# Kernel tuning notes

Hardware: AMD Instinct MI355X
Metric: run time of the kernel (lower is better)

## Reference

```python
import jax, jax.numpy as jnp
import numpy as np

NE, NT, NC, D, NR = 100000, 1024, 128, 128, 500
H, E, L_GCN = 8, 4, 2
B, DEG = 512, 8
NSRC = B * DEG
NNZ_E2T, NNZ_T2C, NNZ_E2C = 1000000, 50000, 500000
TAU, DECAY, CLW = 0.5, 1e-4, 0.1
N_NODES = NE + NT + NC


def setup_inputs() -> dict:
    ks = iter(jax.random.split(jax.random.key(0), 64))
    def n(shape, s=0.05):
        return jax.random.normal(next(ks), shape, jnp.float32) * s
    def ri(shape, hi):
        return jax.random.randint(next(ks), shape, 0, hi, jnp.int32)
    def u(shape):
        return jax.random.uniform(next(ks), shape, jnp.float32) * 0.01
    T = NT
    return {
        'entity_emb': n((NE, D)), 'type_emb': n((NT, D)), 'cluster_emb': n((NC, D)),
        'relation': n((NR, 2 * D)),
        'ln_g': jnp.ones((D,), jnp.float32), 'ln_b': jnp.zeros((D,), jnp.float32),
        'cl_w1': n((D, D)), 'cl_b1': jnp.zeros((D,), jnp.float32),
        'cl_w2': n((D, D)), 'cl_b2': jnp.zeros((D,), jnp.float32),
        'fc_w': n((2 * D, T)), 'fc_b': jnp.zeros((T,), jnp.float32),
        'wq': n((T, T)), 'bq': jnp.zeros((T,), jnp.float32),
        'wk': n((T, T)), 'bk': jnp.zeros((T,), jnp.float32),
        'wv': n((T, T)), 'bv': jnp.zeros((T,), jnp.float32),
        'wo': n((T, T)), 'bo': jnp.zeros((T,), jnp.float32),
        'gate_w': n((T, E)), 'exp_w': n((E, T, T)), 'exp_b': jnp.zeros((E, T), jnp.float32),
        'e2t_val': u((NNZ_E2T,)), 't2c_val': u((NNZ_T2C,)), 'e2c_val': u((NNZ_E2C,)),
        'e2t_row': ri((NNZ_E2T,), NE + NT), 'e2t_col': ri((NNZ_E2T,), NE + NT),
        't2c_row': ri((NNZ_T2C,), NT + NC), 't2c_col': ri((NNZ_T2C,), NT + NC),
        'e2c_row': ri((NNZ_E2C,), NE + NC), 'e2c_col': ri((NNZ_E2C,), NE + NC),
        'src_ids': ri((NSRC,), N_NODES), 'etype': ri((NSRC,), 2 * NR),
    }


def _light_gcn(ea, eb, row, col, val, na, nb):
    x = jnp.concatenate([ea, eb], axis=0)
    acc = x
    for _ in range(L_GCN):  # fixed small layer count
        x = jax.ops.segment_sum(val[:, None] * x[col], row, num_segments=na + nb)
        acc = acc + x
    m = acc / (L_GCN + 1)
    return m[:na], m[na:]


def _ln(x, g, b):
    mu = x.mean(-1, keepdims=True)
    var = x.var(-1, keepdims=True)
    return (x - mu) * jax.lax.rsqrt(var + 1e-5) * g + b


def _cl_loss(src1, src2, w1, b1, w2, b2):
    def proj(x):
        return jax.nn.elu(x @ w1 + b1) @ w2 + b2
    def norm(x):
        return x / jnp.maximum(jnp.linalg.norm(x, axis=1, keepdims=True), 1e-12)
    z1, z2 = norm(proj(src1)), norm(proj(src2))
    s11 = jnp.exp(z1 @ z1.T / TAU)   # [N,N]
    s12 = jnp.exp(z1 @ z2.T / TAU)
    s22 = jnp.exp(z2 @ z2.T / TAU)
    d12 = jnp.diag(s12)
    l1 = -jnp.log(d12 / (s11.sum(1) + s12.sum(1) - jnp.diag(s11)))
    l2 = -jnp.log(d12 / (s22.sum(1) + s12.sum(0) - jnp.diag(s22)))
    return ((l1 + l2) * 0.5).mean()


def _mha_moe(x, wq, bq, wk, bk, wv, bv, wo, bo, gate_w, exp_w, exp_b):
    # x: [B, DEG, T]; MHA over mailbox axis, then softmax-gated MoE, mean-pool.
    b, l, t = x.shape
    dh = t // H
    q = (x @ wq + bq).reshape(b, l, H, dh)
    k = (x @ wk + bk).reshape(b, l, H, dh)
    v = (x @ wv + bv).reshape(b, l, H, dh)
    attn = jax.nn.softmax(jnp.einsum('blhd,bmhd->bhlm', q, k) / jnp.sqrt(jnp.float32(dh)), axis=-1)
    o = jnp.einsum('bhlm,bmhd->blhd', attn, v).reshape(b, l, t) @ wo + bo
    gate = jax.nn.softmax(o @ gate_w, axis=-1)               # [B,L,E]
    eo = jnp.einsum('blt,etu->bleu', o, exp_w) + exp_b       # [B,L,E,T]
    moe = jnp.einsum('ble,blet->blt', gate, eo)
    return moe.mean(axis=1)                                  # [B,T]


def reference(entity_emb, type_emb, cluster_emb, relation, ln_g, ln_b,
              cl_w1, cl_b1, cl_w2, cl_b2, fc_w, fc_b,
              wq, bq, wk, bk, wv, bv, wo, bo, gate_w, exp_w, exp_b,
              e2t_val, t2c_val, e2c_val,
              e2t_row, e2t_col, t2c_row, t2c_col, e2c_row, e2c_col,
              src_ids, etype):
    e2t_e, e2t_t = _light_gcn(entity_emb, type_emb, e2t_row, e2t_col, e2t_val, NE, NT)
    t2c_t, t2c_c = _light_gcn(type_emb, cluster_emb, t2c_row, t2c_col, t2c_val, NT, NC)
    e2c_e, e2c_c = _light_gcn(entity_emb, cluster_emb, e2c_row, e2c_col, e2c_val, NE, NC)
    # with_norm=True path; dropout is eval-mode identity
    e2t_e, e2t_t = _ln(e2t_e, ln_g, ln_b), _ln(e2t_t, ln_g, ln_b)
    t2c_t, t2c_c = _ln(t2c_t, ln_g, ln_b), _ln(t2c_c, ln_g, ln_b)
    e2c_e, e2c_c = _ln(e2c_e, ln_g, ln_b), _ln(e2c_c, ln_g, ln_b)
    node1 = jnp.concatenate([e2t_e, e2t_t, t2c_c], axis=0)
    node2 = jnp.concatenate([e2c_e, t2c_t, e2c_c], axis=0)
    src1 = node1[src_ids]   # [NSRC, D]
    src2 = node2[src_ids]
    cl = _cl_loss(src1, src2, cl_w1, cl_b1, cl_w2, cl_b2)
    src = jnp.concatenate([src1, src2], axis=-1)  # [NSRC, 2D]
    sign = jnp.where(etype >= NR, -1.0, 1.0).astype(jnp.float32)[:, None]
    rel = relation[etype % NR] * sign
    emb_loss = DECAY * ((src ** 2).sum() + (rel ** 2).sum()) * 0.5 / rel.shape[0]
    aux_loss = CLW * cl + emb_loss
    # update_all: u_add_e message, regular mailbox [B, DEG, 2D]
    msg = jax.nn.relu(src + rel).reshape(B, DEG, 2 * D)
    predict = msg @ fc_w + fc_b                                  # [B, DEG, NT]
    predict = _mha_moe(predict, wq, bq, wk, bk, wv, bv, wo, bo, gate_w, exp_w, exp_b)
    out = jax.nn.sigmoid(predict)                                # [B, NT]
    return out, aux_loss
```

## Files before the change

### kernel.cpp

```cpp
#include <hip/hip_runtime.h>
#include <hip/hip_bf16.h>
#include <cmath>

constexpr int cNE = 100000, cNT = 1024, cNC = 128, cD = 128, cNR = 500;
constexpr int cB = 512, cNSRC = 4096, cT = 1024, cE = 4;
constexpr int cNNZ_E2T = 1000000, cNNZ_T2C = 50000, cNNZ_E2C = 500000;
constexpr float cDECAY = 1e-4f, cCLW = 0.1f;
constexpr int cNN_E2T = cNE + cNT;
constexpr int cNN_E2C = cNE + cNC;
constexpr int cNN_T2C = cNT + cNC;

constexpr size_t F_S1   = 0;
constexpr size_t F_S2   = F_S1 + 524288;
constexpr size_t F_PT   = F_S2 + 524288;
constexpr size_t F_Z1   = F_PT + 524288;
constexpr size_t F_Z2   = F_Z1 + 524288;
constexpr size_t F_MSG  = F_Z2 + 524288;
constexpr size_t F_GATE = F_MSG + 524288;
constexpr size_t F_SCAL = F_GATE + 16384;
constexpr size_t F_RS   = F_SCAL + 64;
constexpr size_t F_D11  = F_RS + 16384;
constexpr size_t F_D12  = F_D11 + 4096;
constexpr size_t F_D22  = F_D12 + 4096;
constexpr size_t F_U    = F_D22 + 4096;
// ... 209 lines not shown
}

__global__ __launch_bounds__(256) void k_gather_slot(
    const int* __restrict__ rowptr, const int* __restrict__ cols, const float* __restrict__ vals,
    const ushort* __restrict__ x1, const int* __restrict__ rep,
    ushort* __restrict__ outc) {
  int i = blockIdx.x * 4 + (threadIdx.x >> 6);
  if (i >= cNSRC) return;
  int r = rep[i];
  if (r < 0) return;
  int lane = threadIdx.x & 63;
  int p0 = rowptr[r], p1 = rowptr[r + 1];
  float ax = 0.f, ay = 0.f;
  int p = p0;
  for (; p + 4 <= p1; p += 4) {
    int c0 = cols[p], c1 = cols[p + 1], c2 = cols[p + 2], c3 = cols[p + 3];
    float v0 = vals[p], v1 = vals[p + 1], v2 = vals[p + 2], v3 = vals[p + 3];
    ushort2 x0 = *reinterpret_cast<const ushort2*>(x1 + (size_t)c0 * cD + lane * 2);
    ushort2 x1v = *reinterpret_cast<const ushort2*>(x1 + (size_t)c1 * cD + lane * 2);
    ushort2 x2 = *reinterpret_cast<const ushort2*>(x1 + (size_t)c2 * cD + lane * 2);
    ushort2 x3 = *reinterpret_cast<const ushort2*>(x1 + (size_t)c3 * cD + lane * 2);
    ax += v0 * bf2f(x0.x) + v1 * bf2f(x1v.x) + v2 * bf2f(x2.x) + v3 * bf2f(x3.x);
    ay += v0 * bf2f(x0.y) + v1 * bf2f(x1v.y) + v2 * bf2f(x2.y) + v3 * bf2f(x3.y);
  }
  for (; p < p1; ++p) {
    int c = cols[p];
    float v = vals[p];
    ushort2 x = *reinterpret_cast<const ushort2*>(x1 + (size_t)c * cD + lane * 2);
    ax += v * bf2f(x.x); ay += v * bf2f(x.y);
  }
  ushort2 o; o.x = f2bf(ax); o.y = f2bf(ay);
  *reinterpret_cast<ushort2*>(outc + (size_t)i * cD + lane * 2) = o;
}

__global__ __launch_bounds__(256) void k_gather_bf(
    const int* __restrict__ rowptr, const int* __restrict__ cols, const float* __restrict__ vals,
    const ushort* __restrict__ x1, int nrows, ushort* __restrict__ out) {
  int r = blockIdx.x * 4 + (threadIdx.x >> 6);
  if (r >= nrows) return;
  int lane = threadIdx.x & 63;
  int p0 = rowptr[r], p1 = rowptr[r + 1];
  float ax = 0.f, ay = 0.f;
  for (int p = p0; p < p1; ++p) {
    int c = cols[p];
    float v = vals[p];
    ushort2 x = *reinterpret_cast<const ushort2*>(x1 + (size_t)c * cD + lane * 2);
    ax += v * bf2f(x.x); ay += v * bf2f(x.y);
  }
  ushort2 o; o.x = f2bf(ax); o.y = f2bf(ay);
  *reinterpret_cast<ushort2*>(out + (size_t)r * cD + lane * 2) = o;
}

__global__ __launch_bounds__(128) void gather_ln(
    const int* __restrict__ ids, int mode,
    const float* __restrict__ ea, const float* __restrict__ eb, int na,
    const ushort* __restrict__ x1, const ushort* __restrict__ x2, const int* __restrict__ slot,
    const float* __restrict__ g, const float* __restrict__ bia, float* __restrict__ dst) {
  __shared__ float shx[2], shy[2];
  int i = blockIdx.x;
  int tid = threadIdx.x;
  int id = ids[i];
  int node = mapNode(mode, id);
  if (node < 0) return;
  const float* x0 = (node < na) ? (ea + (size_t)node * cD) : (eb + (size_t)(node - na) * cD);
  int xi2 = slot ? slot[node] : node;
  float a = (x0[tid] + bf2f(x1[(size_t)node * cD + tid]) + bf2f(x2[(size_t)xi2 * cD + tid]))
            * (1.0f / 3.0f);
  float sx = a, sy = a * a;
#pragma unroll
  for (int off = 32; off > 0; off >>= 1) {
    sx += __shfl_xor(sx, off);
    sy += __shfl_xor(sy, off);
  }
  if ((tid & 63) == 0) { shx[tid >> 6] = sx; shy[tid >> 6] = sy; }
  __syncthreads();
  float s  = shx[0] + shx[1];
  float ss = shy[0] + shy[1];
  float mu = s * (1.0f / 128.0f);
  float var = ss * (1.0f / 128.0f) - mu * mu;
  float y = (a - mu) * rsqrtf(var + 1e-5f) * g[tid] + bia[tid];
  dst[(size_t)i * cD + tid] = y;
}

__global__ __launch_bounds__(256) void gemm_bf(
    const ushort* __restrict__ A, const ushort* __restrict__ Bt,
    int N, int K, const float* __restrict__ bias, ushort* __restrict__ Cbf, int epi) {
  __shared__ ushort As[128 * 40];
  __shared__ ushort Bs[128 * 40];
  const int bx = blockIdx.x, by = blockIdx.y;
  const int t = threadIdx.x;
  const int wv = t >> 6, lane = t & 63;
  const int wr = (wv >> 1) * 64, wc = (wv & 1) * 64;
  const int srow = t >> 1, shalf = t & 1;
  const ushort* Ag = A + (size_t)(by * 128 + srow) * K + shalf * 16;
  const ushort* Bg = Bt + (size_t)(bx * 128 + srow) * K + shalf * 16;
  uint4 ra0 = *reinterpret_cast<const uint4*>(Ag);
  uint4 ra1 = *reinterpret_cast<const uint4*>(Ag + 8);
  uint4 rb0 = *reinterpret_cast<const uint4*>(Bg);
  uint4 rb1 = *reinterpret_cast<const uint4*>(Bg + 8);
  f32x4 acc[4][4];
  const f32x4 z4 = {0.f, 0.f, 0.f, 0.f};
#pragma unroll
  for (int i = 0; i < 4; ++i)
#pragma unroll
    for (int j = 0; j < 4; ++j) acc[i][j] = z4;
  const int la = lane & 15, lk = (lane >> 4) * 8;
  const int sdst = srow * 40 + shalf * 16;
  for (int kt = 0; kt < K; kt += 32) {
    __syncthreads();
    *reinterpret_cast<uint4*>(&As[sdst])     = ra0;
    *reinterpret_cast<uint4*>(&As[sdst + 8]) = ra1;
    *reinterpret_cast<uint4*>(&Bs[sdst])     = rb0;
    *reinterpret_cast<uint4*>(&Bs[sdst + 8]) = rb1;
    __syncthreads();
    if (kt + 32 < K) {
      ra0 = *reinterpret_cast<const uint4*>(Ag + kt + 32);
      ra1 = *reinterpret_cast<const uint4*>(Ag + kt + 40);
      rb0 = *reinterpret_cast<const uint4*>(Bg + kt + 32);
      rb1 = *reinterpret_cast<const uint4*>(Bg + kt + 40);
    }
    short8v af[4], bfr[4];
#pragma unroll
    for (int i = 0; i < 4; ++i)
      af[i] = *reinterpret_cast<const short8v*>(&As[(wr + i * 16 + la) * 40 + lk]);
#pragma unroll
    for (int j = 0; j < 4; ++j)
      bfr[j] = *reinterpret_cast<const short8v*>(&Bs[(wc + j * 16 + la) * 40 + lk]);
#pragma unroll
    for (int i = 0; i < 4; ++i)
#pragma unroll
      for (int j = 0; j < 4; ++j)
        acc[i][j] = __builtin_amdgcn_mfma_f32_16x16x32_bf16(af[i], bfr[j], acc[i][j], 0, 0, 0);
  }
  const int r0 = by * 128 + wr + (lane >> 4) * 4;
  const int c0 = bx * 128 + wc + la;
#pragma unroll
  for (int i = 0; i < 4; ++i)
#pragma unroll
    for (int j = 0; j < 4; ++j) {
      int c = c0 + j * 16;
      float bv = bias[c];
#pragma unroll
      for (int q = 0; q < 4; ++q) {
        int r = r0 + i * 16 + q;
        float v = acc[i][j][q] + bv;
        if (epi == 1) v = (v > 0.0f) ? v : expm1f(v);
        Cbf[(size_t)r * N + c] = f2bf(v);
      }
    }
}

__global__ __launch_bounds__(256) void k_gate_pool(
    const ushort* __restrict__ o, const float* __restrict__ gw,
    ushort* __restrict__ ae, float* __restrict__ gsum) {
  __shared__ float os[8][1024];
  __shared__ float lg[8][4];
  __shared__ float gs[8][4];
  const int b = blockIdx.x, t = threadIdx.x;
  for (int u = t; u < 8192; u += 256) {
    int l = u >> 10, d = u & 1023;
    os[l][d] = bf2f(o[(size_t)(b * 8 + l) * 1024 + d]);
  }
  __syncthreads();
  {
    int p = t >> 3, sub = t & 7;
    int l = p >> 2, e = p & 3;
    float s = 0;
    for (int d = sub; d < 1024; d += 8) s += os[l][d] * gw[d * 4 + e];
    s += __shfl_down(s, 4, 8);
    s += __shfl_down(s, 2, 8);
    s += __shfl_down(s, 1, 8);
    if (sub == 0) lg[l][e] = s;
  }
  __syncthreads();
  if (t < 8) {
    float m = fmaxf(fmaxf(lg[t][0], lg[t][1]), fmaxf(lg[t][2], lg[t][3]));
    float e0 = expf(lg[t][0] - m), e1 = expf(lg[t][1] - m);
    float e2 = expf(lg[t][2] - m), e3 = expf(lg[t][3] - m);
    float inv = 1.0f / (e0 + e1 + e2 + e3);
    gs[t][0] = e0 * inv; gs[t][1] = e1 * inv;
    gs[t][2] = e2 * inv; gs[t][3] = e3 * inv;
  }
  __syncthreads();
  if (t < 4) {
    float g = 0;
#pragma unroll
    for (int l = 0; l < 8; ++l) g += gs[l][t];
    gsum[b * 4 + t] = g;
  }
#pragma unroll
  for (int rep = 0; rep < 4; ++rep) {
    int d = t + rep * 256;
    float a0 = 0, a1 = 0, a2 = 0, a3 = 0;
#pragma unroll
    for (int l = 0; l < 8; ++l) {
      float ov = os[l][d];
      a0 += gs[l][0] * ov; a1 += gs[l][1] * ov;
      a2 += gs[l][2] * ov; a3 += gs[l][3] * ov;
    }
    ae[(size_t)0 * 524288 + b * 1024 + d] = f2bf(a0);
    ae[(size_t)1 * 524288 + b * 1024 + d] = f2bf(a1);
    ae[(size_t)2 * 524288 + b * 1024 + d] = f2bf(a2);
    ae[(size_t)3 * 524288 + b * 1024 + d] = f2bf(a3);
  }
}

__global__ __launch_bounds__(256) void gemm_moe2(
    const ushort* __restrict__ AE, const ushort* __restrict__ Bt4,
    const float* __restrict__ expb, const float* __restrict__ gsum,
    float* __restrict__ out) {
  __shared__ ushort As[64 * 40];
  __shared__ ushort Bs[64 * 40];
  const int bx = blockIdx.x, by = blockIdx.y;
  const int t = threadIdx.x;
  const int wv = t >> 6, lane = t & 63;
  const int wr = (wv >> 1) * 32, wc = (wv & 1) * 32;
  const int srow = t >> 2, sq = t & 3;
  const int la = lane & 15, lk = (lane >> 4) * 8;
  const int sdst = srow * 40 + sq * 8;
  f32x4 acc[2][2];
  const f32x4 z4 = {0.f, 0.f, 0.f, 0.f};
  acc[0][0] = z4; acc[0][1] = z4; acc[1][0] = z4; acc[1][1] = z4;
  for (int e = 0; e < 4; ++e) {
    const ushort* Ag = AE + (size_t)e * 524288 + (size_t)(by * 64 + srow) * 1024 + sq * 8;
    const ushort* Bg = Bt4 + (size_t)e * 1048576 + (size_t)(bx * 64 + srow) * 1024 + sq * 8;
    uint4 ra = *reinterpret_cast<const uint4*>(Ag);
    uint4 rb = *reinterpret_cast<const uint4*>(Bg);
    for (int kt = 0; kt < 1024; kt += 32) {
      __syncthreads();
      *reinterpret_cast<uint4*>(&As[sdst]) = ra;
      *reinterpret_cast<uint4*>(&Bs[sdst]) = rb;
      __syncthreads();
      if (kt + 32 < 1024) {
        ra = *reinterpret_cast<const uint4*>(Ag + kt + 32);
        rb = *reinterpret_cast<const uint4*>(Bg + kt + 32);
      }
      short8v af[2], bfr[2];
#pragma unroll
      for (int i = 0; i < 2; ++i)
        af[i] = *reinterpret_cast<const short8v*>(&As[(wr + i * 16 + la) * 40 + lk]);
#pragma unroll
      for (int j = 0; j < 2; ++j)
        bfr[j] = *reinterpret_cast<const short8v*>(&Bs[(wc + j * 16 + la) * 40 + lk]);
#pragma unroll
      for (int i = 0; i < 2; ++i)
#pragma unroll
        for (int j = 0; j < 2; ++j)
          acc[i][j] = __builtin_amdgcn_mfma_f32_16x16x32_bf16(af[i], bfr[j], acc[i][j], 0, 0, 0);
    }
  }
  const int r0 = by * 64 + wr + (lane >> 4) * 4;
  const int c0 = bx * 64 + wc + la;
#pragma unroll
  for (int i = 0; i < 2; ++i)
#pragma unroll
    for (int q = 0; q < 4; ++q) {
      int r = r0 + i * 16 + q;
      float4 gv = *reinterpret_cast<const float4*>(gsum + r * 4);
#pragma unroll
      for (int j = 0; j < 2; ++j) {
        int c = c0 + j * 16;
        float bias = gv.x * expb[c] + gv.y * expb[1024 + c] +
                     gv.z * expb[2048 + c] + gv.w * expb[3072 + c];
        float s = (acc[i][j][q] + bias) * 0.125f;
        out[(size_t)r * 1024 + c] = 1.0f / (1.0f + expf(-s));
      }
    }
}

__global__ __launch_bounds__(256) void gram_sym(
    const ushort* __restrict__ W, float* __restrict__ rsum,
    float* __restrict__ d11, float* __restrict__ d12, float* __restrict__ d22) {
  __shared__ ushort As[128 * 40];
  __shared__ ushort Bs[128 * 40];
  int tt = blockIdx.x, bi = 0, cnt = 64;
  while (tt >= cnt) { tt -= cnt; ++bi; --cnt; }
  int bj = bi + tt;
  const bool diag = (bi == bj);
  const int t = threadIdx.x;
  const int wv = t >> 6, lane = t & 63;
  const int wr = (wv >> 1) * 64, wc = (wv & 1) * 64;
  const int srow = t >> 1, shalf = t & 1;
  const ushort* Ag = W + (size_t)(bi * 128 + srow) * 128 + shalf * 16;
  const ushort* Bg = W + (size_t)(bj * 128 + srow) * 128 + shalf * 16;
  uint4 ra0 = *reinterpret_cast<const uint4*>(Ag);
  uint4 ra1 = *reinterpret_cast<const uint4*>(Ag + 8);
  uint4 rb0 = *reinterpret_cast<const uint4*>(Bg);
  uint4 rb1 = *reinterpret_cast<const uint4*>(Bg + 8);
  f32x4 acc[4][4];
  const f32x4 z4 = {0.f, 0.f, 0.f, 0.f};
#pragma unroll
  for (int i = 0; i < 4; ++i)
#pragma unroll
    for (int j = 0; j < 4; ++j) acc[i][j] = z4;
  const int la = lane & 15, lk = (lane >> 4) * 8;
  const int sdst = srow * 40 + shalf * 16;
  for (int kt = 0; kt < 128; kt += 32) {
    __syncthreads();
    *reinterpret_cast<uint4*>(&As[sdst])     = ra0;
    *reinterpret_cast<uint4*>(&As[sdst + 8]) = ra1;
    *reinterpret_cast<uint4*>(&Bs[sdst])     = rb0;
    *reinterpret_cast<uint4*>(&Bs[sdst + 8]) = rb1;
    __syncthreads();
    if (kt + 32 < 128) {
      ra0 = *reinterpret_cast<const uint4*>(Ag + kt + 32);
      ra1 = *reinterpret_cast<const uint4*>(Ag + kt + 40);
      rb0 = *reinterpret_cast<const uint4*>(Bg + kt + 32);
      rb1 = *reinterpret_cast<const uint4*>(Bg + kt + 40);
    }
    short8v af[4], bfr[4];
#pragma unroll
    for (int i = 0; i < 4; ++i)
      af[i] = *reinterpret_cast<const short8v*>(&As[(wr + i * 16 + la) * 40 + lk]);
#pragma unroll
    for (int j = 0; j < 4; ++j)
      bfr[j] = *reinterpret_cast<const short8v*>(&Bs[(wc + j * 16 + la) * 40 + lk]);
#pragma unroll
    for (int i = 0; i < 4; ++i)
#pragma unroll
      for (int j = 0; j < 4; ++j)
        acc[i][j] = __builtin_amdgcn_mfma_f32_16x16x32_bf16(af[i], bfr[j], acc[i][j], 0, 0, 0);
  }
  const int r0 = bi * 128 + wr + (lane >> 4) * 4;
  const int c0 = bj * 128 + wc + la;
  constexpr float K2 = 2.8853900817779268f;
  float rs[4][4];
  float cs[4] = {0.f, 0.f, 0.f, 0.f};
#pragma unroll
  for (int i = 0; i < 4; ++i)
#pragma unroll
    for (int q = 0; q < 4; ++q) rs[i][q] = 0.f;
#pragma unroll
  for (int i = 0; i < 4; ++i)
#pragma unroll
    for (int j = 0; j < 4; ++j)
#pragma unroll
      for (int q = 0; q < 4; ++q) {
        int r = r0 + i * 16 + q;
        int c = c0 + j * 16;
        float e = exp2f(K2 * acc[i][j][q]);
        rs[i][q] += e;
        cs[j] += e;
        if (c == r)        { if (r < 4096) d11[r] = e; else d22[r - 4096] = e; }
        if (c == r + 4096) d12[r] = e;
      }
#pragma unroll
  for (int m = 1; m < 16; m <<= 1)
#pragma unroll
    for (int i = 0; i < 4; ++i)
#pragma unroll
      for (int q = 0; q < 4; ++q) rs[i][q] += __shfl_xor(rs[i][q], m);
  float* rowdst = rsum + ((bj >= 32) ? 8192 : 0);
  if (la == 0) {
#pragma unroll
    for (int i = 0; i < 4; ++i)
#pragma unroll
      for (int q = 0; q < 4; ++q) atomAdd(&rowdst[r0 + i * 16 + q], rs[i][q]);
  }
  if (!diag) {
#pragma unroll
    for (int j = 0; j < 4; ++j) {
      cs[j] += __shfl_xor(cs[j], 16);
      cs[j] += __shfl_xor(cs[j], 32);
    }
    float* coldst = rsum + ((bi >= 32) ? 8192 : 0);
    if ((lane >> 4) == 0) {
#pragma unroll
      for (int j = 0; j < 4; ++j) atomAdd(&coldst[c0 + j * 16], cs[j]);
    }
  }
}

__global__ __launch_bounds__(256) void cl_row(
    const float* __restrict__ rsum, const float* __restrict__ d11,
    const float* __restrict__ d12, const float* __restrict__ d22,
    float* __restrict__ cl_sum) {
  __shared__ float sh[256];
  int i = blockIdx.x * 256 + threadIdx.x;
  float denA = rsum[i] + rsum[8192 + i] - d11[i];
  float denB = rsum[8192 + 4096 + i] + rsum[4096 + i] - d22[i];
  float l = 0.5f * (logf(denA) + logf(denB)) - logf(d12[i]);
  float s = blockReduce256(l, sh, threadIdx.x);
  if (threadIdx.x == 0) atomAdd(cl_sum, s);
}

__global__ __launch_bounds__(256) void k_wt_bt(const float* __restrict__ W,
                                               ushort* __restrict__ Bt, int K, int N) {
  __shared__ float tile[32][33];
  int n0 = blockIdx.x * 32, k0 = blockIdx.y * 32;
  int tx = threadIdx.x & 31, ty = threadIdx.x >> 5;
#pragma unroll
  for (int i = 0; i < 4; ++i)
    tile[ty + 8 * i][tx] = W[(size_t)(k0 + ty + 8 * i) * N + n0 + tx];
  __syncthreads();
#pragma unroll
  for (int i = 0; i < 4; ++i)
    Bt[(size_t)(n0 + ty + 8 * i) * K + k0 + tx] = f2bf(tile[tx][ty + 8 * i]);
}

__global__ __launch_bounds__(256) void k_wt_bt_s(const float* __restrict__ Wbase,
                                                 ushort* __restrict__ Btbase, int K, int N) {
  __shared__ float tile[32][33];
  const float* W = Wbase + (size_t)blockIdx.z * K * N;
  ushort* Bt = Btbase + (size_t)blockIdx.z * K * N;
  int n0 = blockIdx.x * 32, k0 = blockIdx.y * 32;
  int tx = threadIdx.x & 31, ty = threadIdx.x >> 5;
#pragma unroll
  for (int i = 0; i < 4; ++i)
    tile[ty + 8 * i][tx] = W[(size_t)(k0 + ty + 8 * i) * N + n0 + tx];
  __syncthreads();
#pragma unroll
  for (int i = 0; i < 4; ++i)
    Bt[(size_t)(n0 + ty + 8 * i) * K + k0 + tx] = f2bf(tile[tx][ty + 8 * i]);
}

__global__ __launch_bounds__(256) void k_wt_bt3(const float* __restrict__ w0,
                                                const float* __restrict__ w1,
                                                const float* __restrict__ w2,
                                                ushort* __restrict__ Btbase, int K, int N) {
  __shared__ float tile[32][33];
  const float* W = (blockIdx.z == 0) ? w0 : (blockIdx.z == 1) ? w1 : w2;
  ushort* Bt = Btbase + (size_t)blockIdx.z * K * N;
  int n0 = blockIdx.x * 32, k0 = blockIdx.y * 32;
  int tx = threadIdx.x & 31, ty = threadIdx.x >> 5;
#pragma unroll
  for (int i = 0; i < 4; ++i)
    tile[ty + 8 * i][tx] = W[(size_t)(k0 + ty + 8 * i) * N + n0 + tx];
  __syncthreads();
#pragma unroll
  for (int i = 0; i < 4; ++i)
    Bt[(size_t)(n0 + ty + 8 * i) * K + k0 + tx] = f2bf(tile[tx][ty + 8 * i]);
}

__global__ __launch_bounds__(256) void k_post_s(
    const float* __restrict__ s1, const float* __restrict__ s2,
    const float* __restrict__ relation, const int* __restrict__ etype,
    ushort* __restrict__ sb, ushort* __restrict__ msg, float* __restrict__ emb_out) {
  __shared__ float sh[256];
  float part = 0.f;
  for (int idx = blockIdx.x * 256 + threadIdx.x; idx < 1048576; idx += 128 * 256) {
    float vs = (idx < 524288) ? s1[idx] : s2[idx - 524288];
    sb[idx] = f2bf(vs);
    int i = idx >> 8, j = idx & 255;
    int et = etype[i];
    float sign = (et >= cNR) ? -1.0f : 1.0f;
    float r = relation[(size_t)(et % cNR) * 256 + j];
    float s = (j < 128) ? s1[(size_t)i * 128 + j] : s2[(size_t)i * 128 + j - 128];
    msg[idx] = f2bf(fmaxf(s + r * sign, 0.0f));
    part += s * s + r * r;
  }
  float tot = blockReduce256(part, sh, threadIdx.x);
  if (threadIdx.x == 0) atomAdd(emb_out, tot);
}

__global__ __launch_bounds__(128) void rownorm_bf2(ushort* __restrict__ w) {
  __shared__ float sh[2];
  int i = blockIdx.x, tid = threadIdx.x;
  float v = bf2f(w[(size_t)i * cD + tid]);
  float ss = v * v;
#pragma unroll
  for (int off = 32; off > 0; off >>= 1) ss += __shfl_xor(ss, off);
  if ((tid & 63) == 0) sh[tid >> 6] = ss;
  __syncthreads();
  float n = fmaxf(sqrtf(sh[0] + sh[1]), 1e-12f);
  w[(size_t)i * cD + tid] = f2bf(v / n);
}
// ... 45 lines not shown
    o[(size_t)(b * 8 + ll) * 1024 + h * 128 + d] = f2bf(acc);
  }
}

__global__ void finalize_k(const float* __restrict__ scal, float* __restrict__ out_aux) {
  float cl = scal[0] * (1.0f / cNSRC);
  float emb = cDECAY * 0.5f * scal[1] * (1.0f / cNSRC);
  out_aux[0] = cCLW * cl + emb;
}

extern "C" void kernel_launch(void* const* d_in, const int* in_sizes, int n_in,
                              void* d_out, int out_size, void* d_ws, size_t ws_size,
                              hipStream_t stream) {
  (void)in_sizes; (void)n_in; (void)out_size; (void)ws_size;
  const float* entity   = (const float*)d_in[0];
  const float* type_e   = (const float*)d_in[1];
  const float* cluster  = (const float*)d_in[2];
  const float* relation = (const float*)d_in[3];
  const float* ln_g  = (const float*)d_in[4];
  const float* ln_b  = (const float*)d_in[5];
  const float* cl_w1 = (const float*)d_in[6];
  const float* cl_b1 = (const float*)d_in[7];
  const float* cl_w2 = (const float*)d_in[8];
  const float* cl_b2 = (const float*)d_in[9];
  const float* fc_w  = (const float*)d_in[10];
  const float* fc_b  = (const float*)d_in[11];
  const float* wq = (const float*)d_in[12];
  const float* bq = (const float*)d_in[13];
  const float* wk = (const float*)d_in[14];
  const float* bk = (const float*)d_in[15];
  const float* wv = (const float*)d_in[16];
  const float* bv = (const float*)d_in[17];
  const float* wo = (const float*)d_in[18];
  const float* bo = (const float*)d_in[19];
  const float* gate_w = (const float*)d_in[20];
  const float* exp_w  = (const float*)d_in[21];
  const float* exp_b  = (const float*)d_in[22];
  const float* e2t_val = (const float*)d_in[23];
  const float* t2c_val = (const float*)d_in[24];
  const float* e2c_val = (const float*)d_in[25];
  const int* e2t_row = (const int*)d_in[26];
  const int* e2t_col = (const int*)d_in[27];
  const int* t2c_row = (const int*)d_in[28];
  const int* t2c_col = (const int*)d_in[29];
  const int* e2c_row = (const int*)d_in[30];
  const int* e2c_col = (const int*)d_in[31];
  const int* src_ids = (const int*)d_in[32];
  const int* etype   = (const int*)d_in[33];

  float* ws = (float*)d_ws;
  float* S1 = ws + F_S1;
  float* S2 = ws + F_S2;
  ushort* Wbf = (ushort*)(ws + F_PT);
  ushort* P1bf = (ushort*)(ws + F_Z1);
  ushort* SBbf = (ushort*)(ws + F_Z2);
  ushort* MSGbf = (ushort*)(ws + F_MSG);
  float* GSUM = ws + F_GATE;
  float* SCAL = ws + F_SCAL;
  float* RS   = ws + F_RS;
  float* BQKV = ws + F_RS;
  float* D11  = ws + F_D11;
  float* D12  = ws + F_D12;
  float* D22  = ws + F_D22;
  ushort* X1F = (ushort*)(ws + G_X1F);
  ushort* X2C = (ushort*)(ws + G_X2C);
  int*   MARK = (int*)(ws + G_X2C);
  int*   SLOT = (int*)(ws + G_SLOT);
  int*   REP  = (int*)(ws + G_REP);
  int*   RP   = (int*)(ws + G_RP);
  int*   FILL = (int*)(ws + G_FILL);
  int*   COLS = (int*)(ws + G_COLS);
  float* VALS = ws + G_VALS;
  ushort* X1T = (ushort*)(ws + G_X1T);
  ushort* X2T = (ushort*)(ws + G_X2T);
  int*   BSUM = (int*)(ws + G_BSUM);
  ushort* EBF = (ushort*)(ws + G_EBF);
  ushort* TBF = (ushort*)(ws + G_TBF);
  ushort* CBF = (ushort*)(ws + G_CBF);
  ushort* PB   = (ushort*)(ws + A_U0);
  ushort* AE   = (ushort*)(ws + A_U0);
  ushort* QKV  = (ushort*)(ws + A_U1);
  ushort* OB   = (ushort*)(ws + A_U1);
  ushort* WBT  = (ushort*)(ws + A_WBT);

  hipMemsetAsync(SCAL, 0, 2 * sizeof(float), stream);
  hipMemsetAsync(RS, 0, (16384 + 3 * 4096) * sizeof(float), stream);

  k_to_bf<<<2048, 256, 0, stream>>>(entity, EBF, cNE * cD / 4);
  k_to_bf<<<128, 256, 0, stream>>>(type_e, TBF, cNT * cD / 4);
  k_to_bf<<<16, 256, 0, stream>>>(cluster, CBF, cNC * cD / 4);

  auto run_gcn_masked = [&](const int* row, const int* col, const float* val, int nnz, int nn,
                            const float* ea_f, const float* eb_f,
                            const ushort* ea_b, const ushort* eb_b, int na, int mode,
                            float* dst) {
    int nb = (nn + 255) / 256;
    int gEdge = (nnz + 255) / 256;
    k_init3<<<nb, 256, 0, stream>>>(SLOT, MARK, FILL, nn);
    k_slot_mark<<<16, 256, 0, stream>>>(src_ids, SLOT, MARK, mode);
    k_mark_edges<<<gEdge, 256, 0, stream>>>(row, col, nnz, SLOT, MARK);
    k_hist<<<gEdge, 256, 0, stream>>>(row, nnz, MARK, FILL);
    k_scan_block<<<nb, 256, 0, stream>>>(FILL, nn, RP, BSUM);
    k_bsum_scan<<<1, 512, 0, stream>>>(BSUM, nb, RP, nn);
    k_scan_add<<<nb, 256, 0, stream>>>(RP, BSUM, nn, FILL);
    k_fill<<<gEdge, 256, 0, stream>>>(row, col, val, nnz, MARK, FILL, COLS, VALS);
    k_rep<<<16, 256, 0, stream>>>(src_ids, SLOT, mode, REP);
    k_gather<<<(nn + 3) / 4, 256, 0, stream>>>(RP, COLS, VALS, ea_b, eb_b, na, nn, MARK, X1F);
    k_gather_slot<<<cNSRC / 4, 256, 0, stream>>>(RP, COLS, VALS, X1F, REP, X2C);
    gather_ln<<<cNSRC, 128, 0, stream>>>(src_ids, mode, ea_f, eb_f, na, X1F, X2C, SLOT,
                                         ln_g, ln_b, dst);
  };

  run_gcn_masked(e2t_row, e2t_col, e2t_val, cNNZ_E2T, cNN_E2T,
                 entity, type_e, EBF, TBF, cNE, 0, S1);
  run_gcn_masked(e2c_row, e2c_col, e2c_val, cNNZ_E2C, cNN_E2C,
                 entity, cluster, EBF, CBF, cNE, 3, S2);

  {
    int nn = cNN_T2C, nb = (nn + 255) / 256, gEdge = (cNNZ_T2C + 255) / 256;
    hipMemsetAsync(FILL, 0, (size_t)nn * sizeof(int), stream);
    k_hist<<<gEdge, 256, 0, stream>>>(t2c_row, cNNZ_T2C, nullptr, FILL);
    k_scan_block<<<nb, 256, 0, stream>>>(FILL, nn, RP, BSUM);
    k_bsum_scan<<<1, 512, 0, stream>>>(BSUM, nb, RP, nn);
    k_scan_add<<<nb, 256, 0, stream>>>(RP, BSUM, nn, FILL);
    k_fill<<<gEdge, 256, 0, stream>>>(t2c_row, t2c_col, t2c_val, cNNZ_T2C, nullptr,
                                      FILL, COLS, VALS);
    k_gather<<<(nn + 3) / 4, 256, 0, stream>>>(RP, COLS, VALS, TBF, CBF, cNT,
                                               nn, nullptr, X1T);
    k_gather_bf<<<(nn + 3) / 4, 256, 0, stream>>>(RP, COLS, VALS, X1T, nn, X2T);
    gather_ln<<<cNSRC, 128, 0, stream>>>(src_ids, 1, type_e, cluster, cNT, X1T, X2T, nullptr,
                                         ln_g, ln_b, S1);
    gather_ln<<<cNSRC, 128, 0, stream>>>(src_ids, 2, type_e, cluster, cNT, X1T, X2T, nullptr,
                                         ln_g, ln_b, S2);
  }

  k_post_s<<<128, 256, 0, stream>>>(S1, S2, relation, etype, SBbf, MSGbf, SCAL + 1);

  ushort* W1T = WBT;
  ushort* W2T = WBT + 16384;
  k_wt_bt<<<dim3(4, 4), 256, 0, stream>>>(cl_w1, W1T, cD, cD);
  k_wt_bt<<<dim3(4, 4), 256, 0, stream>>>(cl_w2, W2T, cD, cD);
  gemm_bf<<<dim3(1, 64), 256, 0, stream>>>(SBbf, W1T, cD, cD, cl_b1, P1bf, 1);
  gemm_bf<<<dim3(1, 64), 256, 0, stream>>>(P1bf, W2T, cD, cD, cl_b2, Wbf, 0);
  rownorm_bf2<<<2 * cNSRC, 128, 0, stream>>>(Wbf);
  gram_sym<<<2080, 256, 0, stream>>>(Wbf, RS, D11, D12, D22);
  cl_row<<<16, 256, 0, stream>>>(RS, D11, D12, D22, SCAL);

  k_wt_bt<<<dim3(cT / 32, 256 / 32), 256, 0, stream>>>(fc_w, WBT, 256, cT);
  gemm_bf<<<dim3(cT / 128, cNSRC / 128), 256, 0, stream>>>(MSGbf, WBT, cT, 256, fc_b, PB, 0);

  k_wt_bt3<<<dim3(32, 32, 3), 256, 0, stream>>>(wq, wk, wv, WBT, cT, cT);
  k_pack_bias<<<12, 256, 0, stream>>>(bq, bk, bv, BQKV);
  gemm_bf<<<dim3(3072 / 128, cNSRC / 128), 256, 0, stream>>>(PB, WBT, 3072, cT, BQKV, QKV, 0);
  mha_attn<<<cB * 8, 64, 0, stream>>>(QKV, PB);
  k_wt_bt<<<dim3(32, 32), 256, 0, stream>>>(wo, WBT, cT, cT);
  gemm_bf<<<dim3(cT / 128, cNSRC / 128), 256, 0, stream>>>(PB, WBT, cT, cT, bo, OB, 0);

  k_gate_pool<<<cB, 256, 0, stream>>>(OB, gate_w, AE, GSUM);
  k_wt_bt_s<<<dim3(32, 32, 4), 256, 0, stream>>>(exp_w, WBT, cT, cT);
  gemm_moe2<<<dim3(16, 8), 256, 0, stream>>>(AE, WBT, exp_b, GSUM, (float*)d_out);

  finalize_k<<<1, 1, 0, stream>>>(SCAL, (float*)d_out + (size_t)cB * cT);
}
```

Baseline: 529.5 us.

## Keep gram A-tile in registers and loop over four B tiles per block

Restructures the symmetric Gram kernel so each block loads its row tile once into registers and then computes up to four column tiles sequentially, with B loads prefetched across tiles. This cuts the block count and removes the repeated A-tile global and LDS loads. In exchange it raises register pressure and gives fewer, longer blocks, which may hurt occupancy and load balance.

Measured after the change: 541.4 us. 2.3% more time.

```diff
diff --git a/kernel.cpp b/kernel.cpp
--- a/kernel.cpp
+++ b/kernel.cpp
@@ -501,105 +501,125 @@
     }
 }
 
-__global__ __launch_bounds__(256) void gram_sym(
+__global__ __launch_bounds__(256) void gram_reg(
     const ushort* __restrict__ W, float* __restrict__ rsum,
     float* __restrict__ d11, float* __restrict__ d12, float* __restrict__ d22) {
-  __shared__ ushort As[128 * 40];
   __shared__ ushort Bs[128 * 40];
-  int tt = blockIdx.x, bi = 0, cnt = 64;
-  while (tt >= cnt) { tt -= cnt; ++bi; --cnt; }
-  int bj = bi + tt;
-  const bool diag = (bi == bj);
+  int rem = blockIdx.x, bi = 0;
+  for (;;) { int ch = (64 - bi + 3) >> 2; if (rem < ch) break; rem -= ch; ++bi; }
+  const int bj0 = bi + (rem << 2);
+  const int bjend = (bj0 + 4 < 64) ? bj0 + 4 : 64;
   const int t = threadIdx.x;
   const int wv = t >> 6, lane = t & 63;
   const int wr = (wv >> 1) * 64, wc = (wv & 1) * 64;
   const int srow = t >> 1, shalf = t & 1;
-  const ushort* Ag = W + (size_t)(bi * 128 + srow) * 128 + shalf * 16;
-  const ushort* Bg = W + (size_t)(bj * 128 + srow) * 128 + shalf * 16;
-  uint4 ra0 = *reinterpret_cast<const uint4*>(Ag);
-  uint4 ra1 = *reinterpret_cast<const uint4*>(Ag + 8);
-  uint4 rb0 = *reinterpret_cast<const uint4*>(Bg);
-  uint4 rb1 = *reinterpret_cast<const uint4*>(Bg + 8);
-  f32x4 acc[4][4];
+  const int la = lane & 15, lk = (lane >> 4) * 8;
+  const int soff = srow * 40 + shalf * 16;
+  constexpr float K2 = 2.8853900817779268f;
   const f32x4 z4 = {0.f, 0.f, 0.f, 0.f};
-#pragma unroll
-  for (int i = 0; i < 4; ++i)
-#pragma unroll
-    for (int j = 0; j < 4; ++j) acc[i][j] = z4;
-  const int la = lane & 15, lk = (lane >> 4) * 8;
-  const int sdst = srow * 40 + shalf * 16;
-  for (int kt = 0; kt < 128; kt += 32) {
-    __syncthreads();
-    *reinterpret_cast<uint4*>(&As[sdst])     = ra0;
-    *reinterpret_cast<uint4*>(&As[sdst + 8]) = ra1;
-    *reinterpret_cast<uint4*>(&Bs[sdst])     = rb0;
-    *reinterpret_cast<uint4*>(&Bs[sdst + 8]) = rb1;
-    __syncthreads();
-    if (kt + 32 < 128) {
-      ra0 = *reinterpret_cast<const uint4*>(Ag + kt + 32);
-      ra1 = *reinterpret_cast<const uint4*>(Ag + kt + 40);
-      rb0 = *reinterpret_cast<const uint4*>(Bg + kt + 32);
-      rb1 = *reinterpret_cast<const uint4*>(Bg + kt + 40);
+
+  short8v af[4][4];
+  {
+    const ushort* Ag = W + (size_t)(bi * 128 + srow) * 128 + shalf * 16;
+#pragma unroll
+    for (int kc = 0; kc < 4; ++kc) {
+      uint4 a0 = *reinterpret_cast<const uint4*>(Ag + kc * 32);
+      uint4 a1 = *reinterpret_cast<const uint4*>(Ag + kc * 32 + 8);
+      __syncthreads();
+      *reinterpret_cast<uint4*>(&Bs[soff])     = a0;
+      *reinterpret_cast<uint4*>(&Bs[soff + 8]) = a1;
+      __syncthreads();
+#pragma unroll
+      for (int i = 0; i < 4; ++i)
+        af[kc][i] = *reinterpret_cast<const short8v*>(&Bs[(wr + i * 16 + la) * 40 + lk]);
     }
-    short8v af[4], bfr[4];
+  }
+  const int r0 = bi * 128 + wr + (lane >> 4) * 4;
+
+  uint4 rb0, rb1;
+  {
+    const ushort* Bg = W + (size_t)(bj0 * 128 + srow) * 128 + shalf * 16;
+    rb0 = *reinterpret_cast<const uint4*>(Bg);
+    rb1 = *reinterpret_cast<const uint4*>(Bg + 8);
+  }
+
+  for (int bj = bj0; bj < bjend; ++bj) {
+    f32x4 acc[4][4];
 #pragma unroll
     for (int i = 0; i < 4; ++i)
-      af[i] = *reinterpret_cast<const short8v*>(&As[(wr + i * 16 + la) * 40 + lk]);
-#pragma unroll
-    for (int j = 0; j < 4; ++j)
-      bfr[j] = *reinterpret_cast<const short8v*>(&Bs[(wc + j * 16 + la) * 40 + lk]);
+#pragma unroll
+      for (int j = 0; j < 4; ++j) acc[i][j] = z4;
+#pragma unroll
+    for (int kc = 0; kc < 4; ++kc) {
+      __syncthreads();
+      *reinterpret_cast<uint4*>(&Bs[soff])     = rb0;
+      *reinterpret_cast<uint4*>(&Bs[soff + 8]) = rb1;
+      __syncthreads();
+      if (kc < 3) {
+        const ushort* Bg = W + (size_t)(bj * 128 + srow) * 128 + shalf * 16 + (kc + 1) * 32;
+        rb0 = *reinterpret_cast<const uint4*>(Bg);
+        rb1 = *reinterpret_cast<const uint4*>(Bg + 8);
+      } else if (bj + 1 < bjend) {
+        const ushort* Bg = W + (size_t)((bj + 1) * 128 + srow) * 128 + shalf * 16;
+        rb0 = *reinterpret_cast<const uint4*>(Bg);
+        rb1 = *reinterpret_cast<const uint4*>(Bg + 8);
+      }
+      short8v bfr[4];
+#pragma unroll
+      for (int j = 0; j < 4; ++j)
+        bfr[j] = *reinterpret_cast<const short8v*>(&Bs[(wc + j * 16 + la) * 40 + lk]);
+#pragma unroll
+      for (int i = 0; i < 4; ++i)
+#pragma unroll
+        for (int j = 0; j < 4; ++j)
+          acc[i][j] = __builtin_amdgcn_mfma_f32_16x16x32_bf16(af[kc][i], bfr[j], acc[i][j], 0, 0, 0);
+    }
+    const int c0 = bj * 128 + wc + la;
+    const bool diag = (bj == bi);
+    float rs[4][4];
+    float cs[4] = {0.f, 0.f, 0.f, 0.f};
 #pragma unroll
     for (int i = 0; i < 4; ++i)
 #pragma unroll
+      for (int q = 0; q < 4; ++q) rs[i][q] = 0.f;
+#pragma unroll
+    for (int i = 0; i < 4; ++i)
+#pragma unroll
       for (int j = 0; j < 4; ++j)
-        acc[i][j] = __builtin_amdgcn_mfma_f32_16x16x32_bf16(af[i], bfr[j], acc[i][j], 0, 0, 0);
-  }
-  const int r0 = bi * 128 + wr + (lane >> 4) * 4;
-  const int c0 = bj * 128 + wc + la;
-  constexpr float K2 = 2.8853900817779268f;
-  float rs[4][4];
-  float cs[4] = {0.f, 0.f, 0.f, 0.f};
-#pragma unroll
-  for (int i = 0; i < 4; ++i)
-#pragma unroll
-    for (int q = 0; q < 4; ++q) rs[i][q] = 0.f;
-#pragma unroll
-  for (int i = 0; i < 4; ++i)
-#pragma unroll
-    for (int j = 0; j < 4; ++j)
-#pragma unroll
-      for (int q = 0; q < 4; ++q) {
-        int r = r0 + i * 16 + q;
-        int c = c0 + j * 16;
-        float e = exp2f(K2 * acc[i][j][q]);
-        rs[i][q] += e;
-        cs[j] += e;
-        if (c == r)        { if (r < 4096) d11[r] = e; else d22[r - 4096] = e; }
-        if (c == r + 4096) d12[r] = e;
+#pragma unroll
+        for (int q = 0; q < 4; ++q) {
+          int r = r0 + i * 16 + q;
+          int c = c0 + j * 16;
+          float e = exp2f(K2 * acc[i][j][q]);
+          rs[i][q] += e;
+          cs[j] += e;
+          if (c == r)        { if (r < 4096) d11[r] = e; else d22[r - 4096] = e; }
+          if (c == r + 4096) d12[r] = e;
+        }
+#pragma unroll
+    for (int m = 1; m < 16; m <<= 1)
+#pragma unroll
+      for (int i = 0; i < 4; ++i)
+#pragma unroll
+        for (int q = 0; q < 4; ++q) rs[i][q] += __shfl_xor(rs[i][q], m);
+    float* rowdst = rsum + ((bj >= 32) ? 8192 : 0);
+    if (la == 0) {
+#pragma unroll
+      for (int i = 0; i < 4; ++i)
+#pragma unroll
+        for (int q = 0; q < 4; ++q) atomAdd(&rowdst[r0 + i * 16 + q], rs[i][q]);
+    }
+    if (!diag) {
+#pragma unroll
+      for (int j = 0; j < 4; ++j) {
+        cs[j] += __shfl_xor(cs[j], 16);
+        cs[j] += __shfl_xor(cs[j], 32);
       }
-#pragma unroll
-  for (int m = 1; m < 16; m <<= 1)
-#pragma unroll
-    for (int i = 0; i < 4; ++i)
-#pragma unroll
-      for (int q = 0; q < 4; ++q) rs[i][q] += __shfl_xor(rs[i][q], m);
-  float* rowdst = rsum + ((bj >= 32) ? 8192 : 0);
-  if (la == 0) {
-#pragma unroll
-    for (int i = 0; i < 4; ++i)
-#pragma unroll
-      for (int q = 0; q < 4; ++q) atomAdd(&rowdst[r0 + i * 16 + q], rs[i][q]);
-  }
-  if (!diag) {
-#pragma unroll
-    for (int j = 0; j < 4; ++j) {
-      cs[j] += __shfl_xor(cs[j], 16);
-      cs[j] += __shfl_xor(cs[j], 32);
-    }
-    float* coldst = rsum + ((bi >= 32) ? 8192 : 0);
-    if ((lane >> 4) == 0) {
-#pragma unroll
-      for (int j = 0; j < 4; ++j) atomAdd(&coldst[c0 + j * 16], cs[j]);
+      float* coldst = rsum + ((bi >= 32) ? 8192 : 0);
+      if ((lane >> 4) == 0) {
+#pragma unroll
+        for (int j = 0; j < 4; ++j) atomAdd(&coldst[c0 + j * 16], cs[j]);
+      }
     }
   }
 }
@@ -887,7 +907,7 @@
   gemm_bf<<<dim3(1, 64), 256, 0, stream>>>(SBbf, W1T, cD, cD, cl_b1, P1bf, 1);
   gemm_bf<<<dim3(1, 64), 256, 0, stream>>>(P1bf, W2T, cD, cD, cl_b2, Wbf, 0);
   rownorm_bf2<<<2 * cNSRC, 128, 0, stream>>>(Wbf);
-  gram_sym<<<2080, 256, 0, stream>>>(Wbf, RS, D11, D12, D22);
+  gram_reg<<<544, 256, 0, stream>>>(Wbf, RS, D11, D12, D22);
   cl_row<<<16, 256, 0, stream>>>(RS, D11, D12, D22, SCAL);
 
   k_wt_bt<<<dim3(cT / 32, 256 / 32), 256, 0, stream>>>(fc_w, WBT, 256, cT);
```

## Fuse contrastive gram kernel with QKV GEMM into one launch

Applied to the files above, without the earlier changes.

The contrastive-loss gram kernel (2080 tiles) and the QKV projection GEMM (768 tiles) are merged into one kernel that dispatches on block index, so the two independent workloads run together across CUs. This is meant to fill the idle CUs and tail of each kernel and to remove one launch boundary. The QKV bias buffer is moved to a new workspace offset, presumably so it does not alias buffers the gram work still uses. The cost is a larger kernel with shared LDS sizing, and the gram work can now delay QKV completion.

After: 534.0 us. About the same (+0.9%).

```diff
diff --git a/kernel.cpp b/kernel.cpp
--- a/kernel.cpp
+++ b/kernel.cpp
@@ -315,12 +315,10 @@
   dst[(size_t)i * cD + tid] = y;
 }
 
-__global__ __launch_bounds__(256) void gemm_bf(
+__device__ __forceinline__ void gemm_bf_body(
+    ushort* As, ushort* Bs, int bx, int by,
     const ushort* __restrict__ A, const ushort* __restrict__ Bt,
     int N, int K, const float* __restrict__ bias, ushort* __restrict__ Cbf, int epi) {
-  __shared__ ushort As[128 * 40];
-  __shared__ ushort Bs[128 * 40];
-  const int bx = blockIdx.x, by = blockIdx.y;
   const int t = threadIdx.x;
   const int wv = t >> 6, lane = t & 63;
   const int wr = (wv >> 1) * 64, wc = (wv & 1) * 64;
@@ -381,6 +379,145 @@
         Cbf[(size_t)r * N + c] = f2bf(v);
       }
     }
+}
+
+__global__ __launch_bounds__(256) void gemm_bf(
+    const ushort* __restrict__ A, const ushort* __restrict__ Bt,
+    int N, int K, const float* __restrict__ bias, ushort* __restrict__ Cbf, int epi) {
+  __shared__ ushort As[128 * 40];
+  __shared__ ushort Bs[128 * 40];
+  gemm_bf_body(As, Bs, blockIdx.x, blockIdx.y, A, Bt, N, K, bias, Cbf, epi);
+}
+
+__device__ __forceinline__ void gram_body(
+    ushort* As, ushort* Bs, int tileIdx,
+    const ushort* __restrict__ W, float* __restrict__ rsum,
+    float* __restrict__ d11, float* __restrict__ d12, float* __restrict__ d22) {
+  int tt = tileIdx, bi = 0, cnt = 64;
+  while (tt >= cnt) { tt -= cnt; ++bi; --cnt; }
+  int bj = bi + tt;
+  const bool diag = (bi == bj);
+  const int t = threadIdx.x;
+  const int wv = t >> 6, lane = t & 63;
+  const int wr = (wv >> 1) * 64, wc = (wv & 1) * 64;
+  const int srow = t >> 1, shalf = t & 1;
+  const ushort* Ag = W + (size_t)(bi * 128 + srow) * 128 + shalf * 16;
+  const ushort* Bg = W + (size_t)(bj * 128 + srow) * 128 + shalf * 16;
+  uint4 ra0 = *reinterpret_cast<const uint4*>(Ag);
+  uint4 ra1 = *reinterpret_cast<const uint4*>(Ag + 8);
+  uint4 rb0 = *reinterpret_cast<const uint4*>(Bg);
+  uint4 rb1 = *reinterpret_cast<const uint4*>(Bg + 8);
+  f32x4 acc[4][4];
+  const f32x4 z4 = {0.f, 0.f, 0.f, 0.f};
+#pragma unroll
+  for (int i = 0; i < 4; ++i)
+#pragma unroll
+    for (int j = 0; j < 4; ++j) acc[i][j] = z4;
+  const int la = lane & 15, lk = (lane >> 4) * 8;
+  const int sdst = srow * 40 + shalf * 16;
+  for (int kt = 0; kt < 128; kt += 32) {
+    __syncthreads();
+    *reinterpret_cast<uint4*>(&As[sdst])     = ra0;
+    *reinterpret_cast<uint4*>(&As[sdst + 8]) = ra1;
+    *reinterpret_cast<uint4*>(&Bs[sdst])     = rb0;
+    *reinterpret_cast<uint4*>(&Bs[sdst + 8]) = rb1;
+    __syncthreads();
+    if (kt + 32 < 128) {
+      ra0 = *reinterpret_cast<const uint4*>(Ag + kt + 32);
+      ra1 = *reinterpret_cast<const uint4*>(Ag + kt + 40);
+      rb0 = *reinterpret_cast<const uint4*>(Bg + kt + 32);
+      rb1 = *reinterpret_cast<const uint4*>(Bg + kt + 40);
+    }
+    short8v af[4], bfr[4];
+#pragma unroll
+    for (int i = 0; i < 4; ++i)
+      af[i] = *reinterpret_cast<const short8v*>(&As[(wr + i * 16 + la) * 40 + lk]);
+#pragma unroll
+    for (int j = 0; j < 4; ++j)
+      bfr[j] = *reinterpret_cast<const short8v*>(&Bs[(wc + j * 16 + la) * 40 + lk]);
+#pragma unroll
+    for (int i = 0; i < 4; ++i)
+#pragma unroll
+      for (int j = 0; j < 4; ++j)
+        acc[i][j] = __builtin_amdgcn_mfma_f32_16x16x32_bf16(af[i], bfr[j], acc[i][j], 0, 0, 0);
+  }
+  const int r0 = bi * 128 + wr + (lane >> 4) * 4;
+  const int c0 = bj * 128 + wc + la;
+  constexpr float K2 = 2.8853900817779268f;
+  float rs[4][4];
+  float cs[4] = {0.f, 0.f, 0.f, 0.f};
+#pragma unroll
+  for (int i = 0; i < 4; ++i)
+#pragma unroll
+    for (int q = 0; q < 4; ++q) rs[i][q] = 0.f;
+#pragma unroll
+  for (int i = 0; i < 4; ++i)
+#pragma unroll
+    for (int j = 0; j < 4; ++j)
+#pragma unroll
+      for (int q = 0; q < 4; ++q) {
+        int r = r0 + i * 16 + q;
+        int c = c0 + j * 16;
+        float e = exp2f(K2 * acc[i][j][q]);
+        rs[i][q] += e;
+        cs[j] += e;
+        if (c == r)        { if (r < 4096) d11[r] = e; else d22[r - 4096] = e; }
+        if (c == r + 4096) d12[r] = e;
+      }
+#pragma unroll
+  for (int m = 1; m < 16; m <<= 1)
+#pragma unroll
+    for (int i = 0; i < 4; ++i)
+#pragma unroll
+      for (int q = 0; q < 4; ++q) rs[i][q] += __shfl_xor(rs[i][q], m);
+  float* rowdst = rsum + ((bj >= 32) ? 8192 : 0);
+  if (la == 0) {
+#pragma unroll
+    for (int i = 0; i < 4; ++i)
+#pragma unroll
+      for (int q = 0; q < 4; ++q) atomAdd(&rowdst[r0 + i * 16 + q], rs[i][q]);
+  }
+  if (!diag) {
+#pragma unroll
+    for (int j = 0; j < 4; ++j) {
+      cs[j] += __shfl_xor(cs[j], 16);
+      cs[j] += __shfl_xor(cs[j], 32);
+    }
+    float* coldst = rsum + ((bi >= 32) ? 8192 : 0);
+    if ((lane >> 4) == 0) {
+#pragma unroll
+      for (int j = 0; j < 4; ++j) atomAdd(&coldst[c0 + j * 16], cs[j]);
+    }
+  }
+}
+
+__global__ __launch_bounds__(256) void k_gram_qkv(
+    const ushort* __restrict__ W, float* __restrict__ rsum,
+    float* __restrict__ d11, float* __restrict__ d12, float* __restrict__ d22,
+    const ushort* __restrict__ A, const ushort* __restrict__ Bt,
+    const float* __restrict__ bias, ushort* __restrict__ C) {
+  __shared__ ushort As[128 * 40];
+  __shared__ ushort Bs[128 * 40];
+  int b = blockIdx.x;
+  if (b < 2080) {
+    gram_body(As, Bs, b, W, rsum, d11, d12, d22);
+  } else {
+    int r = b - 2080;
+    gemm_bf_body(As, Bs, r % 24, r / 24, A, Bt, 3072, 1024, bias, C, 0);
+  }
+}
+
+__global__ __launch_bounds__(256) void cl_row(
+    const float* __restrict__ rsum, const float* __restrict__ d11,
+    const float* __restrict__ d12, const float* __restrict__ d22,
+    float* __restrict__ cl_sum) {
+  __shared__ float sh[256];
+  int i = blockIdx.x * 256 + threadIdx.x;
+  float denA = rsum[i] + rsum[8192 + i] - d11[i];
+  float denB = rsum[8192 + 4096 + i] + rsum[4096 + i] - d22[i];
+  float l = 0.5f * (logf(denA) + logf(denB)) - logf(d12[i]);
+  float s = blockReduce256(l, sh, threadIdx.x);
+  if (threadIdx.x == 0) atomAdd(cl_sum, s);
 }
 
 __global__ __launch_bounds__(256) void k_gate_pool(
@@ -499,122 +636,6 @@
         out[(size_t)r * 1024 + c] = 1.0f / (1.0f + expf(-s));
       }
     }
-}
-
-__global__ __launch_bounds__(256) void gram_sym(
-    const ushort* __restrict__ W, float* __restrict__ rsum,
-    float* __restrict__ d11, float* __restrict__ d12, float* __restrict__ d22) {
-  __shared__ ushort As[128 * 40];
-  __shared__ ushort Bs[128 * 40];
-  int tt = blockIdx.x, bi = 0, cnt = 64;
-  while (tt >= cnt) { tt -= cnt; ++bi; --cnt; }
-  int bj = bi + tt;
-  const bool diag = (bi == bj);
-  const int t = threadIdx.x;
-  const int wv = t >> 6, lane = t & 63;
-  const int wr = (wv >> 1) * 64, wc = (wv & 1) * 64;
-  const int srow = t >> 1, shalf = t & 1;
-  const ushort* Ag = W + (size_t)(bi * 128 + srow) * 128 + shalf * 16;
-  const ushort* Bg = W + (size_t)(bj * 128 + srow) * 128 + shalf * 16;
-  uint4 ra0 = *reinterpret_cast<const uint4*>(Ag);
-  uint4 ra1 = *reinterpret_cast<const uint4*>(Ag + 8);
-  uint4 rb0 = *reinterpret_cast<const uint4*>(Bg);
-  uint4 rb1 = *reinterpret_cast<const uint4*>(Bg + 8);
-  f32x4 acc[4][4];
-  const f32x4 z4 = {0.f, 0.f, 0.f, 0.f};
-#pragma unroll
-  for (int i = 0; i < 4; ++i)
-#pragma unroll
-    for (int j = 0; j < 4; ++j) acc[i][j] = z4;
-  const int la = lane & 15, lk = (lane >> 4) * 8;
-  const int sdst = srow * 40 + shalf * 16;
-  for (int kt = 0; kt < 128; kt += 32) {
-    __syncthreads();
-    *reinterpret_cast<uint4*>(&As[sdst])     = ra0;
-    *reinterpret_cast<uint4*>(&As[sdst + 8]) = ra1;
-    *reinterpret_cast<uint4*>(&Bs[sdst])     = rb0;
-    *reinterpret_cast<uint4*>(&Bs[sdst + 8]) = rb1;
-    __syncthreads();
-    if (kt + 32 < 128) {
-      ra0 = *reinterpret_cast<const uint4*>(Ag + kt + 32);
-      ra1 = *reinterpret_cast<const uint4*>(Ag + kt + 40);
-      rb0 = *reinterpret_cast<const uint4*>(Bg + kt + 32);
-      rb1 = *reinterpret_cast<const uint4*>(Bg + kt + 40);
-    }
-    short8v af[4], bfr[4];
-#pragma unroll
-    for (int i = 0; i < 4; ++i)
-      af[i] = *reinterpret_cast<const short8v*>(&As[(wr + i * 16 + la) * 40 + lk]);
-#pragma unroll
-    for (int j = 0; j < 4; ++j)
-      bfr[j] = *reinterpret_cast<const short8v*>(&Bs[(wc + j * 16 + la) * 40 + lk]);
-#pragma unroll
-    for (int i = 0; i < 4; ++i)
-#pragma unroll
-      for (int j = 0; j < 4; ++j)
-        acc[i][j] = __builtin_amdgcn_mfma_f32_16x16x32_bf16(af[i], bfr[j], acc[i][j], 0, 0, 0);
-  }
-  const int r0 = bi * 128 + wr + (lane >> 4) * 4;
-  const int c0 = bj * 128 + wc + la;
-  constexpr float K2 = 2.8853900817779268f;
-  float rs[4][4];
-  float cs[4] = {0.f, 0.f, 0.f, 0.f};
-#pragma unroll
-  for (int i = 0; i < 4; ++i)
-#pragma unroll
-    for (int q = 0; q < 4; ++q) rs[i][q] = 0.f;
-#pragma unroll
-  for (int i = 0; i < 4; ++i)
-#pragma unroll
-    for (int j = 0; j < 4; ++j)
-#pragma unroll
-      for (int q = 0; q < 4; ++q) {
-        int r = r0 + i * 16 + q;
-        int c = c0 + j * 16;
-        float e = exp2f(K2 * acc[i][j][q]);
-        rs[i][q] += e;
-        cs[j] += e;
-        if (c == r)        { if (r < 4096) d11[r] = e; else d22[r - 4096] = e; }
-        if (c == r + 4096) d12[r] = e;
-      }
-#pragma unroll
-  for (int m = 1; m < 16; m <<= 1)
-#pragma unroll
-    for (int i = 0; i < 4; ++i)
-#pragma unroll
-      for (int q = 0; q < 4; ++q) rs[i][q] += __shfl_xor(rs[i][q], m);
-  float* rowdst = rsum + ((bj >= 32) ? 8192 : 0);
-  if (la == 0) {
-#pragma unroll
-    for (int i = 0; i < 4; ++i)
-#pragma unroll
-      for (int q = 0; q < 4; ++q) atomAdd(&rowdst[r0 + i * 16 + q], rs[i][q]);
-  }
-  if (!diag) {
-#pragma unroll
-    for (int j = 0; j < 4; ++j) {
-      cs[j] += __shfl_xor(cs[j], 16);
-      cs[j] += __shfl_xor(cs[j], 32);
-    }
-    float* coldst = rsum + ((bi >= 32) ? 8192 : 0);
-    if ((lane >> 4) == 0) {
-#pragma unroll
-      for (int j = 0; j < 4; ++j) atomAdd(&coldst[c0 + j * 16], cs[j]);
-    }
-  }
-}
-
-__global__ __launch_bounds__(256) void cl_row(
-    const float* __restrict__ rsum, const float* __restrict__ d11,
-    const float* __restrict__ d12, const float* __restrict__ d22,
-    float* __restrict__ cl_sum) {
-  __shared__ float sh[256];
-  int i = blockIdx.x * 256 + threadIdx.x;
-  float denA = rsum[i] + rsum[8192 + i] - d11[i];
-  float denB = rsum[8192 + 4096 + i] + rsum[4096 + i] - d22[i];
-  float l = 0.5f * (logf(denA) + logf(denB)) - logf(d12[i]);
-  float s = blockReduce256(l, sh, threadIdx.x);
-  if (threadIdx.x == 0) atomAdd(cl_sum, s);
 }
 
 __global__ __launch_bounds__(256) void k_wt_bt(const float* __restrict__ W,
@@ -826,6 +847,7 @@
   ushort* QKV  = (ushort*)(ws + A_U1);
   ushort* OB   = (ushort*)(ws + A_U1);
   ushort* WBT  = (ushort*)(ws + A_WBT);
+  float* BQKV2 = ws + F_GATE + 8192;
 
   hipMemsetAsync(SCAL, 0, 2 * sizeof(float), stream);
   hipMemsetAsync(RS, 0, (16384 + 3 * 4096) * sizeof(float), stream);
@@ -887,15 +909,16 @@
   gemm_bf<<<dim3(1, 64), 256, 0, stream>>>(SBbf, W1T, cD, cD, cl_b1, P1bf, 1);
   gemm_bf<<<dim3(1, 64), 256, 0, stream>>>(P1bf, W2T, cD, cD, cl_b2, Wbf, 0);
   rownorm_bf2<<<2 * cNSRC, 128, 0, stream>>>(Wbf);
-  gram_sym<<<2080, 256, 0, stream>>>(Wbf, RS, D11, D12, D22);
-  cl_row<<<16, 256, 0, stream>>>(RS, D11, D12, D22, SCAL);
 
   k_wt_bt<<<dim3(cT / 32, 256 / 32), 256, 0, stream>>>(fc_w, WBT, 256, cT);
   gemm_bf<<<dim3(cT / 128, cNSRC / 128), 256, 0, stream>>>(MSGbf, WBT, cT, 256, fc_b, PB, 0);
 
   k_wt_bt3<<<dim3(32, 32, 3), 256, 0, stream>>>(wq, wk, wv, WBT, cT, cT);
-  k_pack_bias<<<12, 256, 0, stream>>>(bq, bk, bv, BQKV);
-  gemm_bf<<<dim3(3072 / 128, cNSRC / 128), 256, 0, stream>>>(PB, WBT, 3072, cT, BQKV, QKV, 0);
+  k_pack_bias<<<12, 256, 0, stream>>>(bq, bk, bv, BQKV2);
+  k_gram_qkv<<<2080 + 768, 256, 0, stream>>>(Wbf, RS, D11, D12, D22,
+                                             PB, WBT, BQKV2, QKV);
+  cl_row<<<16, 256, 0, stream>>>(RS, D11, D12, D22, SCAL);
+
   mha_attn<<<cB * 8, 64, 0, stream>>>(QKV, PB);
   k_wt_bt<<<dim3(32, 32), 256, 0, stream>>>(wo, WBT, cT, cT);
   gemm_bf<<<dim3(cT / 128, cNSRC / 128), 256, 0, stream>>>(PB, WBT, cT, cT, bo, OB, 0);
```
